# Performance work log

Measured on AMD Instinct MI355X. Metric: run time of the kernel, lower is better.

Reference implementation:

```python
import jax, jax.numpy as jnp
import numpy as np

# ---- constants from the source module ----
N_SAMPLES = 2 ** 15          # exp.n_samples
N_FRAMES = 128
N_HARMONICS = 8
N_EVENTS = 8
FILT_SIZE = 16               # freq_domain_filter_size
N_NOTES = 128                # len(scale)
NYQ = 22050.0 / 2.0          # samplerate nyquist
MIN_F0 = 40.0 / NYQ
F0_SPAN = (3000.0 / NYQ) - MIN_F0
MIN_RES = 0.5
RES_SPAN = 1.0 - MIN_RES
B_EVENTS = 128               # batch(16) * n_events(8)

# packed layout (build_param_slices order):
SL_F0 = slice(0, N_NOTES)                       # 0:128
SL_AMP = slice(N_NOTES + N_FRAMES, N_NOTES + 2 * N_FRAMES)   # 256:384
SL_HAMP = slice(N_NOTES + 2 * N_FRAMES, N_NOTES + 2 * N_FRAMES + N_HARMONICS)  # 384:392
SL_HDEC = slice(N_NOTES + 2 * N_FRAMES + N_HARMONICS, N_NOTES + 2 * N_FRAMES + 2 * N_HARMONICS)  # 392:400
SL_FENV = slice(N_NOTES + 2 * N_FRAMES + 2 * N_HARMONICS, N_NOTES + 2 * N_FRAMES + 2 * N_HARMONICS + FILT_SIZE)  # 400:416


def interp_linear(x, out_size):
    """F.interpolate(..., mode='linear', align_corners=False) on last dim of [B,C,L]."""
    L = x.shape[-1]
    scale = L / out_size
    coords = (jnp.arange(out_size, dtype=x.dtype) + 0.5) * scale - 0.5
    coords = jnp.clip(coords, 0.0, L - 1)
    i0 = jnp.floor(coords).astype(jnp.int32)
    i1 = jnp.minimum(i0 + 1, L - 1)
    w = coords - i0.astype(x.dtype)
    return x[..., i0] * (1.0 - w) + x[..., i1] * w


def setup_inputs() -> dict:
    key = jax.random.key(0)
    k1, k2 = jax.random.split(key)
    packed = jax.random.uniform(k1, (B_EVENTS, N_NOTES + 2 * N_FRAMES + 2 * N_HARMONICS + FILT_SIZE), dtype=jnp.float32)
    # musical-scale center frequencies, normalized by nyquist (geometric 20..3000 Hz)
    hz = 20.0 * (3000.0 / 20.0) ** (np.arange(N_NOTES) / (N_NOTES - 1))
    frequencies = jnp.asarray(hz / NYQ, dtype=jnp.float32)
    global_amp = jnp.full((1,), 5000.0, dtype=jnp.float32)
    osc_amp = jnp.full((1,), 50.0, dtype=jnp.float32)
    noise = jax.random.uniform(k2, (B_EVENTS, 1, N_SAMPLES), dtype=jnp.float32, minval=-1.0, maxval=1.0)
    return {"packed": packed, "frequencies": frequencies, "global_amp": global_amp,
            "osc_amp": osc_amp, "noise": noise}


def reference(packed, frequencies, global_amp, osc_amp, noise):
    B = packed.shape[0]
    # ---- f0 (discrete): softmax over notes, expectation, squared, repeated per frame ----
    f0_scalar = jax.nn.softmax(packed[:, SL_F0], axis=-1) @ frequencies          # [B]
    f0 = (f0_scalar ** 2)[:, None, None] * jnp.ones((1, 1, N_FRAMES), packed.dtype)  # [B,1,F]
    f0 = f0 * NYQ
    f0 = MIN_F0 + f0 * F0_SPAN
    # (the torch line `f0 + f0 + f0_fine` has no assignment -> no effect; f0_fine unused)

    # ---- oscillator bank ----
    harm_factors = jnp.arange(1, N_HARMONICS + 1, dtype=packed.dtype)
    osc = f0 * harm_factors[None, :, None]                      # [B,H,F]
    radians = osc / NYQ * jnp.pi
    radians = jnp.where(radians >= jnp.pi, 0.0, radians)
    radians = interp_linear(radians, N_SAMPLES)                  # [B,H,S]
    osc_bank = jnp.sin(jnp.cumsum(radians, axis=-1)) * osc_amp   # [B,H,S]

    # ---- per-harmonic amplitude recurrence (scan over frames) ----
    harm_decay = MIN_RES + packed[:, SL_HDEC] * RES_SPAN         # [B,H]
    harm_amp = packed[:, SL_HAMP]                                # [B,H]
    amp = packed[:, SL_AMP][:, None, :] * 2.0 - 1.0              # [B,1,F]

    def step(current, amp_i):                                    # current [B,H], amp_i [B,1]
        cur = jnp.maximum(current + amp_i * harm_amp, 0.0)       # clamp(0, inf)
        return cur * harm_decay, cur

    amp_frames = jnp.moveaxis(amp[:, 0, :], 1, 0)[:, :, None]    # [F,B,1]
    _, res = jax.lax.scan(step, jnp.zeros((B, N_HARMONICS), packed.dtype), amp_frames)
    res = jnp.moveaxis(res, 0, 2)                                # [B,H,F]
    res_full = interp_linear(res, N_SAMPLES)                     # [B,H,S]

    # ---- FFT-filtered noise ----
    amp_full = interp_linear(amp, N_SAMPLES)                     # [B,1,S]
    nf = packed[:, SL_FENV][:, None, :]                          # [B,1,16]
    nf = interp_linear(nf, N_SAMPLES // 2)
    nf = jnp.pad(nf, ((0, 0), (0, 0), (0, 1)))                   # [B,1,S//2+1]
    noise_scaled = noise * global_amp
    spec = jnp.fft.rfft(noise_scaled, axis=-1, norm='ortho')
    filt = spec * nf
    noise_out = jnp.fft.irfft(filt, n=N_SAMPLES, axis=-1, norm='ortho')
    noise_out = noise_out * jnp.where(amp_full >= 0, amp_full, 0.2 * amp_full)  # leaky_relu(0.2)

    # ---- combine ----
    x = res_full * osc_bank                                      # [B,H,S]
    x = noise_out / N_HARMONICS + x                              # broadcast [B,1,S]
    x = x.reshape(-1, N_EVENTS, N_HARMONICS, N_SAMPLES)
    x = jnp.sum(x, axis=(1, 2)).reshape(-1, 1, N_SAMPLES)        # [batch,1,S]
    return x
```

## Files before the change

### kernel.cpp

```cpp
#include <hip/hip_runtime.h>
#include <math.h>

#define PCK_STRIDE 416
#define N_SAMPLES  32768
#define FFT_M      16384
#define B_EVENTS   128
#define N_GROUPS   16
#define NT         512
#define PI_F 3.14159265358979323846f
#define RT2H 0.70710678118654752f

#define MAP(i) ((i) + (((i) >> 5) << 2))
#define LDS_N  18432

__device__ inline float filt_at(const float* __restrict__ f, int k) {
    if (k >= FFT_M) return 0.0f;
    float c = ((float)k + 0.5f) * (1.0f / 1024.0f) - 0.5f;
    c = fminf(fmaxf(c, 0.0f), 15.0f);
    int i0 = (int)floorf(c);
    int i1 = min(i0 + 1, 15);
    float w = c - (float)i0;
    return f[i0] * (1.0f - w) + f[i1] * w;
}

template<int L>
__device__ inline void r4_dif_stage(float* re, float* im, int tid) {
    constexpr int q = L >> 2;
    constexpr float ang = -6.28318530717958647692f / (float)L;
    #pragma unroll 2
    for (int s = 0; s < (FFT_M / 4) / NT; ++s) {
        int m = tid + s * NT;
        int t = m & (q - 1);
        int i0 = ((m & ~(q - 1)) << 2) | t;
        int ia = MAP(i0), ib = MAP(i0 + q), ic = MAP(i0 + 2 * q), id = MAP(i0 + 3 * q);
        float ar = re[ia], ai = im[ia];
        float br = re[ib], bi = im[ib];
        float cr = re[ic], ci = im[ic];
        float dr = re[id], di = im[id];
        float s1, c1; __sincosf(ang * (float)t, &s1, &c1);
        float c2 = c1 * c1 - s1 * s1, s2 = 2.0f * c1 * s1;
        float c3 = c2 * c1 - s2 * s1, s3 = c2 * s1 + s2 * c1;
        float s0r = ar + cr, s0i = ai + ci;
        float t1r = br + dr, t1i = bi + di;
        float d0r = ar - cr, d0i = ai - ci;
        float d1r = br - dr, d1i = bi - di;
        re[ia] = s0r + t1r; im[ia] = s0i + t1i;
        float er = s0r - t1r, ei = s0i - t1i;
        re[ib] = er * c2 - ei * s2; im[ib] = er * s2 + ei * c2;
        float fr = d0r + d1i, fi = d0i - d1r;
        re[ic] = fr * c1 - fi * s1; im[ic] = fr * s1 + fi * c1;
        float gr = d0r - d1i, gi = d0i + d1r;
        re[id] = gr * c3 - gi * s3; im[id] = gr * s3 + gi * c3;
    }
    __syncthreads();
}

template<int L>
__device__ inline void r4_dit_stage(float* re, float* im, int tid) {
    constexpr int q = L >> 2;
    constexpr float ang = 6.28318530717958647692f / (float)L;
    #pragma unroll 2
    for (int s = 0; s < (FFT_M / 4) / NT; ++s) {
        int m = tid + s * NT;
        int t = m & (q - 1);
        int i0 = ((m & ~(q - 1)) << 2) | t;
        int ia = MAP(i0), ib = MAP(i0 + q), ic = MAP(i0 + 2 * q), id = MAP(i0 + 3 * q);
        float ar = re[ia], ai = im[ia];
        float br = re[ib], bi = im[ib];
        float cr = re[ic], ci = im[ic];
        float dr = re[id], di = im[id];
        float s1, c1; __sincosf(ang * (float)t, &s1, &c1);
        float c2 = c1 * c1 - s1 * s1, s2 = 2.0f * c1 * s1;
        float tbr = br * c2 - bi * s2, tbi = br * s2 + bi * c2;
        float tdr = dr * c2 - di * s2, tdi = dr * s2 + di * c2;
        float B0r = ar + tbr, B0i = ai + tbi;
        float B1r = ar - tbr, B1i = ai - tbi;
        float B2r = cr + tdr, B2i = ci + tdi;
        float B3r = cr - tdr, B3i = ci - tdi;
        float t0r = B2r * c1 - B2i * s1, t0i = B2r * s1 + B2i * c1;
        float t1r = -B3r * s1 - B3i * c1, t1i = B3r * c1 - B3i * s1;
        re[ia] = B0r + t0r; im[ia] = B0i + t0i;
        re[ib] = B1r + t1r; im[ib] = B1i + t1i;
        re[ic] = B0r - t0r; im[ic] = B0i - t0i;
        re[id] = B1r - t1r; im[id] = B1i - t1i;
    }
    __syncthreads();
}

__global__ __launch_bounds__(NT)
__attribute__((amdgpu_waves_per_eu(2, 2)))
void fft_filter_kernel(
    const float* __restrict__ noise, const float* __restrict__ packed,
    const float* __restrict__ gamp, float* __restrict__ noise_out,
    const float* __restrict__ freqs, float* __restrict__ rW, float* __restrict__ res)
{
    extern __shared__ float smem[];
    float* re = smem;
    float* im = smem + LDS_N;
    float* filt = smem + 2 * LDS_N;
    const int b = blockIdx.x;
    const int tid = threadIdx.x;
    const float g = gamp[0];

    const float2* nz = (const float2*)(noise + (size_t)b * N_SAMPLES);
    #pragma unroll 4
    for (int s = 0; s < 8192 / NT; ++s) {
        int j = tid + s * NT;
        float2 v0 = nz[j];
        float2 v1 = nz[j + 8192];
        float ur = v0.x * g, ui = v0.y * g;
        float wr = v1.x * g, wi = v1.y * g;
        float s1, c1; __sincosf((-PI_F / 8192.0f) * (float)j, &s1, &c1);
        int a0 = MAP(j), a1 = MAP(j + 8192);
        re[a0] = ur + wr; im[a0] = ui + wi;
        float dr = ur - wr, di = ui - wi;
        re[a1] = dr * c1 - di * s1;
        im[a1] = dr * s1 + di * c1;
    }
    if (tid >= 64 && tid < 80) filt[tid - 64] = packed[b * PCK_STRIDE + 400 + (tid - 64)];

    if (tid < 64) {
        const float* row = packed + b * PCK_STRIDE;
        float n0 = row[tid], n1 = row[tid + 64];
        float fq0 = freqs[tid], fq1 = freqs[tid + 64];
        float mx = fmaxf(n0, n1);
        #pragma unroll
        for (int off = 32; off >= 1; off >>= 1) mx = fmaxf(mx, __shfl_xor(mx, off));
        float e0 = __expf(n0 - mx), e1 = __expf(n1 - mx);
        float den = e0 + e1, num = e0 * fq0 + e1 * fq1;
        #pragma unroll
        for (int off = 32; off >= 1; off >>= 1) {
            den += __shfl_xor(den, off);
            num += __shfl_xor(num, off);
        }
        float ampA = row[256 + tid] * 2.0f - 1.0f;
        float ampB = row[320 + tid] * 2.0f - 1.0f;
        int h = tid & 7;
        float ha = row[384 + h];
        float hd = 0.5f + row[392 + h] * 0.5f;
        const float MIN_F0 = 40.0f / 11025.0f;
        const float F0_SPAN = 3000.0f / 11025.0f - 40.0f / 11025.0f;
        float f0s = num / den;
        float f0 = MIN_F0 + f0s * f0s * 11025.0f * F0_SPAN;
        float r = f0 * (float)(h + 1) * (PI_F / 11025.0f);
        if (r >= PI_F) r = 0.0f;
        if (tid < 8) rW[b * 8 + tid] = r;
        float cur = 0.0f;
        float* rr = res + (b * 8 + h) * 128;
        for (int f = 0; f < 64; ++f) {
            float av = __shfl(ampA, f);
            float c = fmaxf(cur + av * ha, 0.0f);
            if (tid < 8) rr[f] = c;
            cur = c * hd;
        }
        for (int f = 0; f < 64; ++f) {
            float av = __shfl(ampB, f);
            float c = fmaxf(cur + av * ha, 0.0f);
            if (tid < 8) rr[64 + f] = c;
            cur = c * hd;
        }
    }
    __syncthreads();

    r4_dif_stage<8192>(re, im, tid);
    r4_dif_stage<2048>(re, im, tid);
    r4_dif_stage<512>(re, im, tid);
    r4_dif_stage<128>(re, im, tid);
    r4_dif_stage<32>(re, im, tid);

    #pragma unroll 2
    for (int s = 0; s < 2048 / NT; ++s) {
        int m = (2048 / NT) * tid + s;
        int a = MAP(8 * m);
        float4 r0 = *(const float4*)(re + a);
        float4 r1 = *(const float4*)(re + a + 4);
        float4 q0 = *(const float4*)(im + a);
        float4 q1 = *(const float4*)(im + a + 4);
        float t0r = r0.x + r1.x, t0i = q0.x + q1.x;
        float u0r = r0.x - r1.x, u0i = q0.x - q1.x;
        float d1r = r0.y - r1.y, d1i = q0.y - q1.y;
        float t1r = r0.y + r1.y, t1i = q0.y + q1.y;
        float u1r = RT2H * (d1r + d1i), u1i = RT2H * (d1i - d1r);
        float t2r = r0.z + r1.z, t2i = q0.z + q1.z;
        float d2r = r0.z - r1.z, d2i = q0.z - q1.z;
        float u2r = d2i, u2i = -d2r;
        float t3r = r0.w + r1.w, t3i = q0.w + q1.w;
        float d3r = r0.w - r1.w, d3i = q0.w - q1.w;
        float u3r = RT2H * (d3i - d3r), u3i = -RT2H * (d3r + d3i);
        float A0r = t0r + t2r, A0i = t0i + t2i;
        float A2r = t0r - t2r, A2i = t0i - t2i;
        float A1r = t1r + t3r, A1i = t1i + t3i;
        float e3r = t1r - t3r, e3i = t1i - t3i;
        float A3r = e3i, A3i = -e3r;
        float B0r = u0r + u2r, B0i = u0i + u2i;
        float B2r = u0r - u2r, B2i = u0i - u2i;
        float B1r = u1r + u3r, B1i = u1i + u3i;
        float f3r = u1r - u3r, f3i = u1i - u3i;
        float B3r = f3i, B3i = -f3r;
        r0.x = A0r + A1r; q0.x = A0i + A1i;
        r0.y = A0r - A1r; q0.y = A0i - A1i;
        r0.z = A2r + A3r; q0.z = A2i + A3i;
        r0.w = A2r - A3r; q0.w = A2i - A3i;
        r1.x = B0r + B1r; q1.x = B0i + B1i;
        r1.y = B0r - B1r; q1.y = B0i - B1i;
        r1.z = B2r + B3r; q1.z = B2i + B3i;
        r1.w = B2r - B3r; q1.w = B2i - B3i;
        *(float4*)(re + a) = r0; *(float4*)(re + a + 4) = r1;
        *(float4*)(im + a) = q0; *(float4*)(im + a + 4) = q1;
    }
    __syncthreads();

    const float invM = 1.0f / (float)FFT_M;
    #pragma unroll 2
    for (int s = 0; s < 8192 / NT; ++s) {
        int jj = (tid + s * NT) << 1;
        if (jj == 0) {
            int p0 = MAP(0);
            float z0r = re[p0], z0i = im[p0];
            float y = 0.5f * filt_at(filt, 0) * (z0r + z0i) * invM;
            re[p0] = y; im[p0] = y;
            int p1 = MAP(1);
            float H = filt_at(filt, 8192) * invM;
            re[p1] *= H; im[p1] *= H;
        } else {
            int k = (int)(__brev((unsigned)jj) >> 18);
            int kq = FFT_M - k;
            int pk = MAP(jj);
            int pq = MAP((int)(__brev((unsigned)kq) >> 18));
            float zkr = re[pk], zki = im[pk];
            float zqr = re[pq], zqi = im[pq];
            float Er = 0.5f * (zkr + zqr), Ei = 0.5f * (zki - zqi);
            float Or = 0.5f * (zki + zqi), Oi = 0.5f * (zqr - zkr);
            float th = (float)k * (PI_F / (float)FFT_M);
            float s1, c1; __sincosf(th, &s1, &c1);
            float ts = -s1;
            float tOr = c1 * Or - ts * Oi;
            float tOi = c1 * Oi + ts * Or;
            float Hk = filt_at(filt, k);
            float Hq = filt_at(filt, kq);
            float Ykr = Hk * (Er + tOr), Yki = Hk * (Ei + tOi);
            float Cr  = Hq * (Er - tOr), Ci  = Hq * (Ei - tOi);
            float Ar = 0.5f * (Ykr + Cr), Ai = 0.5f * (Yki + Ci);
            float Br = 0.5f * (Ykr - Cr), Bi = 0.5f * (Yki - Ci);
            re[pk] = (Ar + ts * Br - c1 * Bi) * invM;
            im[pk] = (Ai + c1 * Br + ts * Bi) * invM;
            re[pq] = (Ar + c1 * Bi - ts * Br) * invM;
            im[pq] = (-Ai + c1 * Br + ts * Bi) * invM;
        }
    }
    __syncthreads();

    #pragma unroll 2
    for (int s = 0; s < 2048 / NT; ++s) {
        int m = (2048 / NT) * tid + s;
        int a = MAP(8 * m);
        float4 r0 = *(const float4*)(re + a);
        float4 r1 = *(const float4*)(re + a + 4);
        float4 q0 = *(const float4*)(im + a);
        float4 q1 = *(const float4*)(im + a + 4);
        float A0r = r0.x + r0.y, A0i = q0.x + q0.y;
        float A1r = r0.x - r0.y, A1i = q0.x - q0.y;
        float A2r = r0.z + r0.w, A2i = q0.z + q0.w;
        float A3r = r0.z - r0.w, A3i = q0.z - q0.w;
        float B0r = r1.x + r1.y, B0i = q1.x + q1.y;
        float B1r = r1.x - r1.y, B1i = q1.x - q1.y;
        float B2r = r1.z + r1.w, B2i = q1.z + q1.w;
        float B3r = r1.z - r1.w, B3i = q1.z - q1.w;
        float t0r = A0r + A2r, t0i = A0i + A2i;
        float t2r = A0r - A2r, t2i = A0i - A2i;
        float w3r = -A3i, w3i = A3r;
        float t1r = A1r + w3r, t1i = A1i + w3i;
        float t3r = A1r - w3r, t3i = A1i - w3i;
        float u0r = B0r + B2r, u0i = B0i + B2i;
        float u2r = B0r - B2r, u2i = B0i - B2i;
        float x3r = -B3i, x3i = B3r;
        float u1r = B1r + x3r, u1i = B1i + x3i;
        float u3r = B1r - x3r, u3i = B1i - x3i;
        float w1r = RT2H * (u1r - u1i), w1i = RT2H * (u1r + u1i);
        float w2r = -u2i,               w2i = u2r;
        float w5r = RT2H * (-u3r - u3i), w5i = RT2H * (u3r - u3i);
        r0.x = t0r + u0r; q0.x = t0i + u0i;
        r1.x = t0r - u0r; q1.x = t0i - u0i;
        r0.y = t1r + w1r; q0.y = t1i + w1i;
        r1.y = t1r - w1r; q1.y = t1i - w1i;
        r0.z = t2r + w2r; q0.z = t2i + w2i;
        r1.z = t2r - w2r; q1.z = t2i - w2i;
        r0.w = t3r + w5r; q0.w = t3i + w5i;
        r1.w = t3r - w5r; q1.w = t3i - w5i;
        *(float4*)(re + a) = r0; *(float4*)(re + a + 4) = r1;
        *(float4*)(im + a) = q0; *(float4*)(im + a + 4) = q1;
    }
    __syncthreads();

    r4_dit_stage<32>(re, im, tid);
    r4_dit_stage<128>(re, im, tid);
    r4_dit_stage<512>(re, im, tid);
    r4_dit_stage<2048>(re, im, tid);
    r4_dit_stage<8192>(re, im, tid);

    float2* oz = (float2*)(noise_out + (size_t)b * N_SAMPLES);
    #pragma unroll 4
    for (int s = 0; s < 8192 / NT; ++s) {
        int j = tid + s * NT;
        int a0 = MAP(j), a1 = MAP(j + 8192);
        float ur = re[a0], ui = im[a0];
        float xr = re[a1], xi = im[a1];
        float s1, c1; __sincosf((PI_F / 8192.0f) * (float)j, &s1, &c1);
        float wr = xr * c1 - xi * s1, wi = xr * s1 + xi * c1;
        oz[j] = make_float2(ur + wr, ui + wi);
        oz[j + 8192] = make_float2(ur - wr, ui - wi);
    }
}

__global__ __launch_bounds__(256) void assemble_kernel(
    const float* __restrict__ packed, const float* __restrict__ rW,
    const float* __restrict__ res, const float* __restrict__ noise_out,
    const float* __restrict__ oamp, float* __restrict__ out)
{
    const int g = blockIdx.y;
    const int chunk = blockIdx.x;
    const int tid = threadIdx.x;
    const int n = chunk * 256 + tid;
    const int fb = chunk - 1;

    __shared__ float s_res[8][8][3];
    __shared__ float s_ampf[8][3];
    __shared__ float s_r[8][8];
    if (tid < 192) {
        int e = tid / 24, rem = tid % 24, h = rem / 3, j = rem % 3;
        int f = min(max(fb + j, 0), 127);
        s_res[e][h][j] = res[((g * 8 + e) * 8 + h) * 128 + f];
    }
    if (tid < 24) {
        int e = tid / 3, j = tid % 3;
        int f = min(max(fb + j, 0), 127);
        s_ampf[e][j] = packed[(g * 8 + e) * PCK_STRIDE + 256 + f] * 2.0f - 1.0f;
    }
    if (tid >= 192 && tid < 256) {
        int u = tid - 192;
        s_r[u / 8][u % 8] = rW[g * 64 + u];
    }
    __syncthreads();

    float coords = ((float)n + 0.5f) * (1.0f / 256.0f) - 0.5f;
    coords = fminf(fmaxf(coords, 0.0f), 127.0f);
    int i0 = (int)floorf(coords);
    float w = coords - (float)i0;
    int j0 = i0 - fb;
    float osc50 = oamp[0];
    float pn = (float)(n + 1);
    float wm = 1.0f - w;

    float acc = 0.0f;
    #pragma unroll
    for (int e = 0; e < 8; ++e) {
        int b = g * 8 + e;
        float nv = noise_out[(size_t)b * N_SAMPLES + n];
        float av = s_ampf[e][j0] * wm + s_ampf[e][j0 + 1] * w;
        float gate = (av >= 0.0f) ? av : 0.2f * av;
        acc += nv * gate;
        float sn, cn; __sincosf(pn * s_r[e][0], &sn, &cn);
        float c2 = 2.0f * cn;
        float shm1 = 0.0f, sh = sn;
        #pragma unroll
        for (int h = 0; h < 8; ++h) {
            float rsv = s_res[e][h][j0] * wm + s_res[e][h][j0 + 1] * w;
            float sv = (s_r[e][h] != 0.0f) ? sh : 0.0f;
            acc += rsv * osc50 * sv;
            float nx = c2 * sh - shm1;
            shm1 = sh; sh = nx;
        }
    }
    out[(size_t)g * N_SAMPLES + n] = acc;
}

extern "C" void kernel_launch(void* const* d_in, const int* in_sizes, int n_in,
                              void* d_out, int out_size, void* d_ws, size_t ws_size,
                              hipStream_t stream) {
    const float* packed = (const float*)d_in[0];
    const float* freqs  = (const float*)d_in[1];
    const float* gamp   = (const float*)d_in[2];
    const float* oamp   = (const float*)d_in[3];
    const float* noise  = (const float*)d_in[4];
    float* out = (float*)d_out;

    float* ws = (float*)d_ws;
    float* noise_out = ws;
    float* res = ws + (size_t)B_EVENTS * N_SAMPLES;
    float* rW  = res + B_EVENTS * 8 * 128;

    fft_filter_kernel<<<B_EVENTS, NT, (2 * LDS_N + 16) * sizeof(float), stream>>>(
        noise, packed, gamp, noise_out, freqs, rW, res);
    assemble_kernel<<<dim3(N_SAMPLES / 256, N_GROUPS), 256, 0, stream>>>(
        packed, rW, res, noise_out, oamp, out);
}
```

Before: 121.8 us.

## Fuse pairs of radix-4 FFT stages into register-resident radix-16 passes

Replaces four radix-4 DIF stages (8192,2048,512,128) and the matching DIT stages with two radix-16 passes each, keeping 16 complex values in registers per thread. This halves the LDS round trips and __syncthreads barriers in the forward and inverse FFTs. It raises register pressure (32 floats of data per thread plus twiddles) under the existing waves_per_eu constraint, which may cause spills or reduced occupancy. The butterfly code is refactored into shared helpers, and the recurrence loops are marked unroll 1.

New measurement: 119.7 us. Within noise of the previous version (-1.7%).

```diff
diff --git a/kernel.cpp b/kernel.cpp
--- a/kernel.cpp
+++ b/kernel.cpp
@@ -12,6 +12,7 @@
 
 #define MAP(i) ((i) + (((i) >> 5) << 2))
 #define LDS_N  18432
+#define LDS_TOTAL (2 * LDS_N + 16)
 
 __device__ inline float filt_at(const float* __restrict__ f, int k) {
     if (k >= FFT_M) return 0.0f;
@@ -21,6 +22,114 @@
     int i1 = min(i0 + 1, 15);
     float w = c - (float)i0;
     return f[i0] * (1.0f - w) + f[i1] * w;
+}
+
+__device__ inline void bf4_dif(float& ar, float& ai, float& br, float& bi,
+                               float& cr, float& ci, float& dr, float& di,
+                               float c1, float s1) {
+    float c2 = c1 * c1 - s1 * s1, s2 = 2.0f * c1 * s1;
+    float c3 = c2 * c1 - s2 * s1, s3 = c2 * s1 + s2 * c1;
+    float s0r = ar + cr, s0i = ai + ci;
+    float t1r = br + dr, t1i = bi + di;
+    float d0r = ar - cr, d0i = ai - ci;
+    float d1r = br - dr, d1i = bi - di;
+    ar = s0r + t1r; ai = s0i + t1i;
+    float er = s0r - t1r, ei = s0i - t1i;
+    br = er * c2 - ei * s2; bi = er * s2 + ei * c2;
+    float fr = d0r + d1i, fi = d0i - d1r;
+    cr = fr * c1 - fi * s1; ci = fr * s1 + fi * c1;
+    float gr = d0r - d1i, gi = d0i + d1r;
+    dr = gr * c3 - gi * s3; di = gr * s3 + gi * c3;
+}
+
+__device__ inline void bf4_dit(float& ar, float& ai, float& br, float& bi,
+                               float& cr, float& ci, float& dr, float& di,
+                               float c1, float s1) {
+    float c2 = c1 * c1 - s1 * s1, s2 = 2.0f * c1 * s1;
+    float tbr = br * c2 - bi * s2, tbi = br * s2 + bi * c2;
+    float tdr = dr * c2 - di * s2, tdi = dr * s2 + di * c2;
+    float B0r = ar + tbr, B0i = ai + tbi;
+    float B1r = ar - tbr, B1i = ai - tbi;
+    float B2r = cr + tdr, B2i = ci + tdi;
+    float B3r = cr - tdr, B3i = ci - tdi;
+    float t0r = B2r * c1 - B2i * s1, t0i = B2r * s1 + B2i * c1;
+    float t1r = -B3r * s1 - B3i * c1, t1i = B3r * c1 - B3i * s1;
+    ar = B0r + t0r; ai = B0i + t0i;
+    br = B1r + t1r; bi = B1i + t1i;
+    cr = B0r - t0r; ci = B0i - t0i;
+    dr = B1r - t1r; di = B1i - t1i;
+}
+
+template<int L>
+__device__ inline void r16_dif_stage(float* re, float* im, int tid) {
+    constexpr int q = L >> 4;
+    constexpr float ang = -6.28318530717958647692f / (float)L;
+    const float C16_1 = 0.9238795325112867f, S16_1 = -0.3826834323650898f;
+    const float C16_2 = 0.7071067811865476f, S16_2 = -0.7071067811865476f;
+    const float C16_3 = 0.3826834323650898f, S16_3 = -0.9238795325112867f;
+    #pragma unroll 1
+    for (int s = 0; s < (FFT_M / 16) / NT; ++s) {
+        int m = tid + s * NT;
+        int t = m & (q - 1);
+        int i0 = ((m & ~(q - 1)) << 4) | t;
+        float xr[16], xi[16];
+        #pragma unroll
+        for (int j = 0; j < 16; ++j) { int a = MAP(i0 + j * q); xr[j] = re[a]; xi[j] = im[a]; }
+        float sv, cv; __sincosf(ang * (float)t, &sv, &cv);
+        float cA0 = cv, sA0 = sv;
+        float cA1 = cv * C16_1 - sv * S16_1, sA1 = sv * C16_1 + cv * S16_1;
+        float cA2 = cv * C16_2 - sv * S16_2, sA2 = sv * C16_2 + cv * S16_2;
+        float cA3 = cv * C16_3 - sv * S16_3, sA3 = sv * C16_3 + cv * S16_3;
+        bf4_dif(xr[0], xi[0], xr[4], xi[4], xr[8],  xi[8],  xr[12], xi[12], cA0, sA0);
+        bf4_dif(xr[1], xi[1], xr[5], xi[5], xr[9],  xi[9],  xr[13], xi[13], cA1, sA1);
+        bf4_dif(xr[2], xi[2], xr[6], xi[6], xr[10], xi[10], xr[14], xi[14], cA2, sA2);
+        bf4_dif(xr[3], xi[3], xr[7], xi[7], xr[11], xi[11], xr[15], xi[15], cA3, sA3);
+        float c2v = cv * cv - sv * sv, s2v = 2.0f * cv * sv;
+        float c4 = c2v * c2v - s2v * s2v, s4 = 2.0f * c2v * s2v;
+        bf4_dif(xr[0],  xi[0],  xr[1],  xi[1],  xr[2],  xi[2],  xr[3],  xi[3],  c4, s4);
+        bf4_dif(xr[4],  xi[4],  xr[5],  xi[5],  xr[6],  xi[6],  xr[7],  xi[7],  c4, s4);
+        bf4_dif(xr[8],  xi[8],  xr[9],  xi[9],  xr[10], xi[10], xr[11], xi[11], c4, s4);
+        bf4_dif(xr[12], xi[12], xr[13], xi[13], xr[14], xi[14], xr[15], xi[15], c4, s4);
+        #pragma unroll
+        for (int j = 0; j < 16; ++j) { int a = MAP(i0 + j * q); re[a] = xr[j]; im[a] = xi[j]; }
+    }
+    __syncthreads();
+}
+
+template<int L>
+__device__ inline void r16_dit_stage(float* re, float* im, int tid) {
+    constexpr int q = L >> 4;
+    constexpr float ang = 6.28318530717958647692f / (float)L;
+    const float C16_1 = 0.9238795325112867f, S16_1 = 0.3826834323650898f;
+    const float C16_2 = 0.7071067811865476f, S16_2 = 0.7071067811865476f;
+    const float C16_3 = 0.3826834323650898f, S16_3 = 0.9238795325112867f;
+    #pragma unroll 1
+    for (int s = 0; s < (FFT_M / 16) / NT; ++s) {
+        int m = tid + s * NT;
+        int t = m & (q - 1);
+        int i0 = ((m & ~(q - 1)) << 4) | t;
+        float xr[16], xi[16];
+        #pragma unroll
+        for (int j = 0; j < 16; ++j) { int a = MAP(i0 + j * q); xr[j] = re[a]; xi[j] = im[a]; }
+        float sv, cv; __sincosf(ang * (float)t, &sv, &cv);
+        float c2v = cv * cv - sv * sv, s2v = 2.0f * cv * sv;
+        float c4 = c2v * c2v - s2v * s2v, s4 = 2.0f * c2v * s2v;
+        bf4_dit(xr[0],  xi[0],  xr[1],  xi[1],  xr[2],  xi[2],  xr[3],  xi[3],  c4, s4);
+        bf4_dit(xr[4],  xi[4],  xr[5],  xi[5],  xr[6],  xi[6],  xr[7],  xi[7],  c4, s4);
+        bf4_dit(xr[8],  xi[8],  xr[9],  xi[9],  xr[10], xi[10], xr[11], xi[11], c4, s4);
+        bf4_dit(xr[12], xi[12], xr[13], xi[13], xr[14], xi[14], xr[15], xi[15], c4, s4);
+        float cA0 = cv, sA0 = sv;
+        float cA1 = cv * C16_1 - sv * S16_1, sA1 = sv * C16_1 + cv * S16_1;
+        float cA2 = cv * C16_2 - sv * S16_2, sA2 = sv * C16_2 + cv * S16_2;
+        float cA3 = cv * C16_3 - sv * S16_3, sA3 = sv * C16_3 + cv * S16_3;
+        bf4_dit(xr[0], xi[0], xr[4], xi[4], xr[8],  xi[8],  xr[12], xi[12], cA0, sA0);
+        bf4_dit(xr[1], xi[1], xr[5], xi[5], xr[9],  xi[9],  xr[13], xi[13], cA1, sA1);
+        bf4_dit(xr[2], xi[2], xr[6], xi[6], xr[10], xi[10], xr[14], xi[14], cA2, sA2);
+        bf4_dit(xr[3], xi[3], xr[7], xi[7], xr[11], xi[11], xr[15], xi[15], cA3, sA3);
+        #pragma unroll
+        for (int j = 0; j < 16; ++j) { int a = MAP(i0 + j * q); re[a] = xr[j]; im[a] = xi[j]; }
+    }
+    __syncthreads();
 }
 
 template<int L>
@@ -38,19 +147,11 @@
         float cr = re[ic], ci = im[ic];
         float dr = re[id], di = im[id];
         float s1, c1; __sincosf(ang * (float)t, &s1, &c1);
-        float c2 = c1 * c1 - s1 * s1, s2 = 2.0f * c1 * s1;
-        float c3 = c2 * c1 - s2 * s1, s3 = c2 * s1 + s2 * c1;
-        float s0r = ar + cr, s0i = ai + ci;
-        float t1r = br + dr, t1i = bi + di;
-        float d0r = ar - cr, d0i = ai - ci;
-        float d1r = br - dr, d1i = bi - di;
-        re[ia] = s0r + t1r; im[ia] = s0i + t1i;
-        float er = s0r - t1r, ei = s0i - t1i;
-        re[ib] = er * c2 - ei * s2; im[ib] = er * s2 + ei * c2;
-        float fr = d0r + d1i, fi = d0i - d1r;
-        re[ic] = fr * c1 - fi * s1; im[ic] = fr * s1 + fi * c1;
-        float gr = d0r - d1i, gi = d0i + d1r;
-        re[id] = gr * c3 - gi * s3; im[id] = gr * s3 + gi * c3;
+        bf4_dif(ar, ai, br, bi, cr, ci, dr, di, c1, s1);
+        re[ia] = ar; im[ia] = ai;
+        re[ib] = br; im[ib] = bi;
+        re[ic] = cr; im[ic] = ci;
+        re[id] = dr; im[id] = di;
     }
     __syncthreads();
 }
@@ -70,19 +171,11 @@
         float cr = re[ic], ci = im[ic];
         float dr = re[id], di = im[id];
         float s1, c1; __sincosf(ang * (float)t, &s1, &c1);
-        float c2 = c1 * c1 - s1 * s1, s2 = 2.0f * c1 * s1;
-        float tbr = br * c2 - bi * s2, tbi = br * s2 + bi * c2;
-        float tdr = dr * c2 - di * s2, tdi = dr * s2 + di * c2;
-        float B0r = ar + tbr, B0i = ai + tbi;
-        float B1r = ar - tbr, B1i = ai - tbi;
-        float B2r = cr + tdr, B2i = ci + tdi;
-        float B3r = cr - tdr, B3i = ci - tdi;
-        float t0r = B2r * c1 - B2i * s1, t0i = B2r * s1 + B2i * c1;
-        float t1r = -B3r * s1 - B3i * c1, t1i = B3r * c1 - B3i * s1;
-        re[ia] = B0r + t0r; im[ia] = B0i + t0i;
-        re[ib] = B1r + t1r; im[ib] = B1i + t1i;
-        re[ic] = B0r - t0r; im[ic] = B0i - t0i;
-        re[id] = B1r - t1r; im[id] = B1i - t1i;
+        bf4_dit(ar, ai, br, bi, cr, ci, dr, di, c1, s1);
+        re[ia] = ar; im[ia] = ai;
+        re[ib] = br; im[ib] = bi;
+        re[ic] = cr; im[ic] = ci;
+        re[id] = dr; im[id] = di;
     }
     __syncthreads();
 }
@@ -147,12 +240,14 @@
         if (tid < 8) rW[b * 8 + tid] = r;
         float cur = 0.0f;
         float* rr = res + (b * 8 + h) * 128;
+        #pragma unroll 1
         for (int f = 0; f < 64; ++f) {
             float av = __shfl(ampA, f);
             float c = fmaxf(cur + av * ha, 0.0f);
             if (tid < 8) rr[f] = c;
             cur = c * hd;
         }
+        #pragma unroll 1
         for (int f = 0; f < 64; ++f) {
             float av = __shfl(ampB, f);
             float c = fmaxf(cur + av * ha, 0.0f);
@@ -162,10 +257,8 @@
     }
     __syncthreads();
 
-    r4_dif_stage<8192>(re, im, tid);
-    r4_dif_stage<2048>(re, im, tid);
-    r4_dif_stage<512>(re, im, tid);
-    r4_dif_stage<128>(re, im, tid);
+    r16_dif_stage<8192>(re, im, tid);
+    r16_dif_stage<512>(re, im, tid);
     r4_dif_stage<32>(re, im, tid);
 
     #pragma unroll 2
@@ -293,10 +386,8 @@
     __syncthreads();
 
     r4_dit_stage<32>(re, im, tid);
-    r4_dit_stage<128>(re, im, tid);
-    r4_dit_stage<512>(re, im, tid);
-    r4_dit_stage<2048>(re, im, tid);
-    r4_dit_stage<8192>(re, im, tid);
+    r16_dit_stage<512>(re, im, tid);
+    r16_dit_stage<8192>(re, im, tid);
 
     float2* oz = (float2*)(noise_out + (size_t)b * N_SAMPLES);
     #pragma unroll 4
@@ -389,7 +480,7 @@
     float* res = ws + (size_t)B_EVENTS * N_SAMPLES;
     float* rW  = res + B_EVENTS * 8 * 128;
 
-    fft_filter_kernel<<<B_EVENTS, NT, (2 * LDS_N + 16) * sizeof(float), stream>>>(
+    fft_filter_kernel<<<B_EVENTS, NT, LDS_TOTAL * sizeof(float), stream>>>(
         noise, packed, gamp, noise_out, freqs, rW, res);
     assemble_kernel<<<dim3(N_SAMPLES / 256, N_GROUPS), 256, 0, stream>>>(
         packed, rW, res, noise_out, oamp, out);
```
